# Optimization experiments

Measured on AMD Instinct MI355X. Metric: run time of the kernel, lower is better.

## Reference

```python
import jax, jax.numpy as jnp
import numpy as np

D_MODEL = 768
D_FF = 3072
N_EXPERTS = 4
BATCH, SEQ = 8, 2048


def setup_inputs() -> dict:
    key = jax.random.key(0)
    ks = jax.random.split(key, 8)
    s_in = 1.0 / np.sqrt(D_MODEL)
    s_ff = 1.0 / np.sqrt(D_FF)
    return {
        "hidden_states": jax.random.normal(ks[0], (BATCH, SEQ, D_MODEL), jnp.float32),
        "Wg": jax.random.normal(ks[1], (D_MODEL, N_EXPERTS), jnp.float32) * s_in,
        "bg": jnp.zeros((N_EXPERTS,), jnp.float32),
        "W1": jax.random.normal(ks[2], (N_EXPERTS, D_MODEL, D_FF), jnp.float32) * s_in,
        "b1": jnp.zeros((N_EXPERTS, D_FF), jnp.float32),
        "W2": jax.random.normal(ks[3], (N_EXPERTS, D_FF, D_MODEL), jnp.float32) * s_ff,
        "b2": jnp.zeros((N_EXPERTS, D_MODEL), jnp.float32),
    }


def reference(hidden_states, Wg, bg, W1, b1, W2, b2):
    """Switch-Transformer top-1 MoE FFN (no token dropping).

    router: softmax(x @ Wg + bg); each token goes to argmax expert,
    expert FFN: gelu(x @ W1[e] + b1[e]) @ W2[e] + b2[e],
    output scaled by the winning route probability.
    """
    B, S, D = hidden_states.shape
    xt = hidden_states.reshape(-1, D)                      # [T, D]
    logits = xt @ Wg + bg                                  # [T, E]
    probs = jax.nn.softmax(logits, axis=-1)
    gate = jnp.max(probs, axis=-1)                         # [T]
    route = jnp.argmax(probs, axis=-1)                     # [T] int

    out = jnp.zeros_like(xt)
    for e in range(W1.shape[0]):                           # small fixed expert count
        mask = (route == e).astype(xt.dtype)[:, None]      # [T, 1]
        h = jax.nn.gelu(xt @ W1[e] + b1[e])                # [T, d_ff]
        y = h @ W2[e] + b2[e]                              # [T, D]
        out = out + mask * y
    out = out * gate[:, None]
    return out.reshape(B, S, D)
```

## Files before the change

### kernel.cpp

```cpp
#include <hip/hip_runtime.h>
#include <hip/hip_bf16.h>

#define T_TOK 16384
#define DMODEL 768
#define DFF 3072
#define NEXP 4
#define ROWPAD 512
#define BK 64

typedef __attribute__((ext_vector_type(8))) short bf16x8;
typedef __attribute__((ext_vector_type(4))) float f32x4;

__device__ __forceinline__ void gl_lds16(const void* g, void* l) {
  __builtin_amdgcn_global_load_lds(
      (const __attribute__((address_space(1))) unsigned int*)g,
      (__attribute__((address_space(3))) unsigned int*)l, 16, 0, 0);
}

__device__ __forceinline__ short f2bf(float f) {
  union { float f; unsigned u; } v; v.f = f;
  unsigned r = v.u + 0x7fff + ((v.u >> 16) & 1);
  return (short)(r >> 16);
}

__device__ __forceinline__ float gelu_f(float x) {
  const float c = 0.7978845608028654f;
  float z = c * (x + 0.044715f * x * x * x);
  z = fminf(fmaxf(z, -15.f), 15.f);
  float e = __expf(-2.f * z);
  return 0.5f * x * (1.f + (1.f - e) / (1.f + e));
}


__device__ __forceinline__ int expert_aoff(const int* counts, int e) {
  int off = 0;
  for (int i = 0; i < e; ++i) off += (counts[i] + 127) & ~127;
  return off;
}

__global__ void route_kernel(const float* __restrict__ x, const float* __restrict__ Wg,
                             const float* __restrict__ bg, int* __restrict__ route,
                             float* __restrict__ gate) {
  int t = blockIdx.x * 4 + (threadIdx.x >> 6);
  int l = threadIdx.x & 63;
  const float* xr = x + (size_t)t * DMODEL;
  float s0 = 0.f, s1 = 0.f, s2 = 0.f, s3 = 0.f;
#pragma unroll
  for (int i = 0; i < DMODEL / 64; ++i) {
    int d = l + i * 64;
    float xv = xr[d];
    float4 w = *((const float4*)Wg + d);
    s0 += xv * w.x; s1 += xv * w.y; s2 += xv * w.z; s3 += xv * w.w;
  }
#pragma unroll
  for (int off = 32; off; off >>= 1) {
    s0 += __shfl_xor(s0, off);
    s1 += __shfl_xor(s1, off);
    s2 += __shfl_xor(s2, off);
    s3 += __shfl_xor(s3, off);
  }
  if (l == 0) {
    float lg[4] = { s0 + bg[0], s1 + bg[1], s2 + bg[2], s3 + bg[3] };
    int best = 0; float m = lg[0];
#pragma unroll
    for (int e = 1; e < 4; ++e) if (lg[e] > m) { m = lg[e]; best = e; }
    float s = 0.f;
#pragma unroll
    for (int e = 0; e < 4; ++e) s += __expf(lg[e] - m);
    route[t] = best;
    gate[t] = 1.0f / s;
  }
}

__global__ void bucket_kernel(const int* __restrict__ route, int* __restrict__ counts,
                              int* __restrict__ perm) {
  __shared__ int wcnt[4][NEXP];
  __shared__ int wpre[4][NEXP];
  __shared__ int base[NEXP];
  int tid = threadIdx.x;
  int t = blockIdx.x * 256 + tid;
  int w = tid >> 6, l = tid & 63;
  int r = route[t];
  int lanepre = 0;
  unsigned long long lower = (l == 0) ? 0ull : (~0ull >> (64 - l));
#pragma unroll
  for (int e = 0; e < NEXP; ++e) {
    unsigned long long m = __ballot(r == e);
    if (l == 0) wcnt[w][e] = (int)__popcll(m);
    if (r == e) lanepre = (int)__popcll(m & lower);
  }
  __syncthreads();
  if (tid < NEXP) {
    int s = 0;
#pragma unroll
    for (int ww = 0; ww < 4; ++ww) { wpre[ww][tid] = s; s += wcnt[ww][tid]; }
    base[tid] = atomicAdd(&counts[tid], s);
  }
  __syncthreads();
  int pos = base[r] + wpre[w][r] + lanepre;
  perm[r * T_TOK + pos] = t;
}

__global__ void gather_kernel(const float* __restrict__ x, const int* __restrict__ counts,
                              const int* __restrict__ perm, const float* __restrict__ gate,
                              short* __restrict__ xg, int* __restrict__ tokg,
                              float* __restrict__ gateg) {
  int e = blockIdx.y;
  int cnt = counts[e];
  int pos = blockIdx.x * 8 + (threadIdx.x >> 5);
  if (pos >= cnt) return;
  int off = expert_aoff(counts, e);
  int t = perm[e * T_TOK + pos];
  int g = off + pos;
  int l = threadIdx.x & 31;
  const float* src = x + (size_t)t * DMODEL;
  short* dst = xg + (size_t)g * DMODEL;
  int sw = g & 7;
#pragma unroll
  for (int i = 0; i < 3; ++i) {
    int c = l + 32 * i;
    float4 a = *((const float4*)src + c * 2);
    float4 b = *((const float4*)src + c * 2 + 1);
    bf16x8 v;
    v[0] = f2bf(a.x); v[1] = f2bf(a.y); v[2] = f2bf(a.z); v[3] = f2bf(a.w);
    v[4] = f2bf(b.x); v[5] = f2bf(b.y); v[6] = f2bf(b.z); v[7] = f2bf(b.w);
    int cs = (c & ~7) | ((c & 7) ^ sw);
    *(bf16x8*)(dst + cs * 8) = v;
  }
  if (l == 0) { tokg[g] = t; gateg[g] = gate[t]; }
}

__global__ void transpose_kernel(const float* __restrict__ src, short* __restrict__ dst,
                                 int K, int N) {
  __shared__ float lds[64 * 65];
  int e = blockIdx.z;
  int k0 = blockIdx.x * 64, n0 = blockIdx.y * 64;
  const float* s = src + (size_t)e * K * N;
  short* d = dst + (size_t)e * N * K;
#pragma unroll
  for (int i = 0; i < 16; ++i) {
    int idx = threadIdx.x + i * 256;
    int kk = idx >> 6, nn = idx & 63;
    lds[kk * 65 + nn] = s[(size_t)(k0 + kk) * N + n0 + nn];
  }
  __syncthreads();
#pragma unroll
  for (int i = 0; i < 2; ++i) {
    int cid = threadIdx.x + i * 256;
    int nn = cid >> 3, uu = cid & 7;
    int n = n0 + nn;
    bf16x8 v;
#pragma unroll
    for (int j = 0; j < 8; ++j) v[j] = f2bf(lds[(uu * 8 + j) * 65 + nn]);
    int cs = (k0 >> 3) + (uu ^ (n & 7));
    *(bf16x8*)(d + (size_t)n * K + cs * 8) = v;
  }
}

__device__ __forceinline__ int xcd_chunk(int orig, int nwg) {
  int q = nwg >> 3, r = nwg & 7, xcd = orig & 7;
  return (xcd < r ? xcd * (q + 1) : r * (q + 1) + (xcd - r) * q) + (orig >> 3);
}

__device__ __forceinline__ bool decode_expert(const int* counts, int gm,
                                              int& e, int& off, int& cnt, int& m0) {
  int c0 = counts[0], c1 = counts[1], c2 = counts[2], c3 = counts[3];
  int mb0 = (c0 + 127) >> 7, mb1 = (c1 + 127) >> 7, mb2 = (c2 + 127) >> 7, mb3 = (c3 + 127) >> 7;
  int o1 = (c0 + 127) & ~127, o2 = o1 + ((c1 + 127) & ~127), o3 = o2 + ((c2 + 127) & ~127);
  if (gm < mb0)                        { e = 0; off = 0;  cnt = c0; m0 = gm << 7; return true; }
  if (gm < mb0 + mb1)                  { e = 1; off = o1; cnt = c1; m0 = (gm - mb0) << 7; return true; }
  if (gm < mb0 + mb1 + mb2)            { e = 2; off = o2; cnt = c2; m0 = (gm - mb0 - mb1) << 7; return true; }
  if (gm < mb0 + mb1 + mb2 + mb3)      { e = 3; off = o3; cnt = c3; m0 = (gm - mb0 - mb1 - mb2) << 7; return true; }
  return false;
}

__global__ __launch_bounds__(256, 4)
void gemm1_kernel(const short* __restrict__ xg, const short* __restrict__ w1t,
                  const float* __restrict__ b1, const int* __restrict__ counts,
                  short* __restrict__ h, int FFC, int chunk, int MBG) {
  __shared__ __align__(16) short smem[2 * 128 * 64];
  short* sA = smem;
  short* sB = smem + 128 * 64;
  int L = xcd_chunk(blockIdx.x, gridDim.x);
  int np = L / MBG, gm = L - np * MBG;
  int e, off, cnt, m0;
  if (!decode_expert(counts, gm, e, off, cnt, m0)) return;
  int n0c = np * 128;
  int n0g = chunk * FFC + n0c;

  const char* Abase = (const char*)(xg + (size_t)(off + m0) * DMODEL);
  const char* Bbase = (const char*)(w1t + (size_t)e * DFF * DMODEL + (size_t)n0g * DMODEL);

  int tid = threadIdx.x, wid = tid >> 6, lane = tid & 63;
  int wm = wid >> 1, wn = wid & 1;
  int l15 = lane & 15, u4 = lane >> 4;

  f32x4 acc[4][4];
#pragma unroll
  for (int i = 0; i < 4; ++i)
#pragma unroll
    for (int j = 0; j < 4; ++j) acc[i][j] = (f32x4){0.f, 0.f, 0.f, 0.f};

  for (int kt = 0; kt < DMODEL / BK; ++kt) {
    int kb = kt * 128;
#pragma unroll
    for (int r = 0; r < 4; ++r) {
      int o = wid * 1024 + r * 4096 + lane * 16;
      int row = o >> 7, b = o & 127;
      gl_lds16(Abase + (size_t)row * (DMODEL * 2) + kb + b, (char*)sA + wid * 1024 + r * 4096);
      gl_lds16(Bbase + (size_t)row * (DMODEL * 2) + kb + b, (char*)sB + wid * 1024 + r * 4096);
    }
    __syncthreads();
#pragma unroll
    for (int ks = 0; ks < 2; ++ks) {
      int u = ks * 4 + u4;
      int slot8 = (u ^ (l15 & 7)) << 3;
      bf16x8 af[4], bfr[4];
#pragma unroll
      for (int mi = 0; mi < 4; ++mi)
        af[mi] = *(const bf16x8*)&sA[(wm * 64 + mi * 16 + l15) * 64 + slot8];
#pragma unroll
      for (int ni = 0; ni < 4; ++ni)
        bfr[ni] = *(const bf16x8*)&sB[(wn * 64 + ni * 16 + l15) * 64 + slot8];
#pragma unroll
      for (int mi = 0; mi < 4; ++mi)
#pragma unroll
        for (int ni = 0; ni < 4; ++ni)
          acc[mi][ni] = __builtin_amdgcn_mfma_f32_16x16x32_bf16(af[mi], bfr[ni], acc[mi][ni], 0, 0, 0);
    }
    __syncthreads();
  }

  float bbs[4];
#pragma unroll
  for (int ni = 0; ni < 4; ++ni) bbs[ni] = b1[e * DFF + n0g + wn * 64 + ni * 16 + l15];
  short* bounce = smem;
#pragma unroll
  for (int mi = 0; mi < 4; ++mi)
#pragma unroll
    for (int ni = 0; ni < 4; ++ni) {
      f32x4 v = acc[mi][ni];
      int col = wn * 64 + ni * 16 + l15;
      int c = col >> 3;
#pragma unroll
      for (int qq = 0; qq < 4; ++qq) {
        int rl = wm * 64 + mi * 16 + u4 * 4 + qq;
        int swc = (c & ~7) | ((c & 7) ^ (rl & 7));
        bounce[rl * 128 + swc * 8 + (col & 7)] = f2bf(gelu_f(v[qq] + bbs[ni]));
      }
    }
  __syncthreads();
#pragma unroll
  for (int it = 0; it < 8; ++it) {
    int cc = tid + it * 256;
    int rw = cc >> 4, sl = cc & 15;
    int grow = m0 + rw;
    if (grow < cnt) {
      size_t g = (size_t)off + grow;
      *(bf16x8*)((char*)h + (g * FFC + n0c) * 2 + sl * 16) =
          *(const bf16x8*)((char*)bounce + cc * 16);
    }
  }
}

__global__ __launch_bounds__(512, 4)
void gemm2_kernel(const short* __restrict__ h, const short* __restrict__ w2t,
                  const float* __restrict__ b2, const int* __restrict__ counts,
                  const int* __restrict__ tokg, const float* __restrict__ gateg,
                  float* __restrict__ out, int FFC, int chunk, int nchunks, int MBG) {
  __shared__ __align__(16) short sA[128 * 64];
  __shared__ __align__(16) short sB[256 * 64];
  int L = xcd_chunk(blockIdx.x, gridDim.x);
  int np = L / MBG, gm = L - np * MBG;
  int e, off, cnt, m0;
  if (!decode_expert(counts, gm, e, off, cnt, m0)) return;
  int n0 = np * 256;

  const char* Ar = (const char*)(h + (size_t)(off + m0) * FFC);
  const char* Br = (const char*)(w2t + (size_t)e * DMODEL * DFF + (size_t)n0 * DFF + (size_t)chunk * FFC);

  int tid = threadIdx.x, wid = tid >> 6, lane = tid & 63;
  int wm = wid >> 2, wn = wid & 3;
  int l15 = lane & 15, u4 = lane >> 4;

  f32x4 acc[4][4];
#pragma unroll
  for (int i = 0; i < 4; ++i)
#pragma unroll
    for (int j = 0; j < 4; ++j) acc[i][j] = (f32x4){0.f, 0.f, 0.f, 0.f};

  for (int kt = 0; kt < FFC / BK; ++kt) {
    int kb = kt * 128;
#pragma unroll
    for (int p = 0; p < 2; ++p) {
      int cc = tid + p * 512;
      int row = cc >> 3, b = (cc & 7) * 16;
      gl_lds16(Ar + (size_t)row * (FFC * 2) + kb + b, (char*)sA + (wid * 64 + p * 512) * 16);
    }
#pragma unroll
    for (int p = 0; p < 4; ++p) {
      int cc = tid + p * 512;
      int row = cc >> 3, b = (cc & 7) * 16;
      gl_lds16(Br + (size_t)row * (DFF * 2) + kb + b, (char*)sB + (wid * 64 + p * 512) * 16);
    }
    __syncthreads();
#pragma unroll
    for (int ks = 0; ks < 2; ++ks) {
      int u = ks * 4 + u4;
      int slot8 = (u ^ (l15 & 7)) << 3;
      bf16x8 af[4], bfr[4];
#pragma unroll
      for (int mi = 0; mi < 4; ++mi)
        af[mi] = *(const bf16x8*)&sA[(wm * 64 + mi * 16 + l15) * 64 + slot8];
#pragma unroll
      for (int ni = 0; ni < 4; ++ni)
        bfr[ni] = *(const bf16x8*)&sB[(wn * 64 + ni * 16 + l15) * 64 + slot8];
#pragma unroll
      for (int mi = 0; mi < 4; ++mi)
#pragma unroll
        for (int ni = 0; ni < 4; ++ni)
          acc[mi][ni] = __builtin_amdgcn_mfma_f32_16x16x32_bf16(af[mi], bfr[ni], acc[mi][ni], 0, 0, 0);
    }
    __syncthreads();
  }

#pragma unroll
  for (int ni = 0; ni < 4; ++ni) {
    int colg = n0 + wn * 64 + ni * 16 + l15;
    float bb = b2[e * DMODEL + colg];
#pragma unroll
    for (int mi = 0; mi < 4; ++mi) {
      f32x4 v = acc[mi][ni];
#pragma unroll
      for (int qq = 0; qq < 4; ++qq) {
        int ml = m0 + wm * 64 + mi * 16 + u4 * 4 + qq;
        if (ml < cnt) {
          int g = off + ml;
          float* op = out + (size_t)tokg[g] * DMODEL + colg;
          float pv = v[qq];
          if (chunk == 0 && nchunks > 1) {
            *op = pv;
          } else if (chunk < nchunks - 1) {
            *op += pv;
          } else {
            float prev = (nchunks > 1) ? *op : 0.f;
            *op = (prev + pv + bb) * gateg[g];
          }
        }
      }
    }
  }
}

extern "C" void kernel_launch(void* const* d_in, const int* in_sizes, int n_in,
                              void* d_out, int out_size, void* d_ws, size_t ws_size,
                              hipStream_t stream) {
  (void)in_sizes; (void)n_in; (void)out_size;
  const float* x  = (const float*)d_in[0];
  const float* Wg = (const float*)d_in[1];
  const float* bg = (const float*)d_in[2];
  const float* W1 = (const float*)d_in[3];
  const float* b1 = (const float*)d_in[4];
  const float* W2 = (const float*)d_in[5];
  const float* b2 = (const float*)d_in[6];
  float* out = (float*)d_out;
  char* ws = (char*)d_ws;

  size_t cur = 0;
  auto take = [&](size_t bytes) -> size_t {
    cur = (cur + 255) & ~(size_t)255;
    size_t r = cur; cur += bytes; return r;
  };
  size_t o_counts = take(64);
  size_t o_perm  = take((size_t)NEXP * T_TOK * 4);
  size_t o_route = take((size_t)T_TOK * 4);
  size_t o_gate  = take((size_t)T_TOK * 4);
  size_t o_tokg  = take((size_t)(T_TOK + ROWPAD) * 4);
  size_t o_gateg = take((size_t)(T_TOK + ROWPAD) * 4);
  size_t o_w1t   = take((size_t)NEXP * DFF * DMODEL * 2);
  size_t o_w2t   = take((size_t)NEXP * DMODEL * DFF * 2);
  size_t o_xg    = take((size_t)(T_TOK + ROWPAD) * DMODEL * 2);
  cur = (cur + 255) & ~(size_t)255;
  size_t o_h = cur;

  int FFC = 384;
  const int cands[4] = {3072, 1536, 768, 384};
  for (int i = 0; i < 4; ++i) {
    if (o_h + (size_t)(T_TOK + ROWPAD) * cands[i] * 2 <= ws_size) { FFC = cands[i]; break; }
  }

  int*   counts = (int*)(ws + o_counts);
  int*   perm   = (int*)(ws + o_perm);
  int*   routeb = (int*)(ws + o_route);
  float* gate   = (float*)(ws + o_gate);
  int*   tokg   = (int*)(ws + o_tokg);
  float* gateg  = (float*)(ws + o_gateg);
  short* w1t    = (short*)(ws + o_w1t);
  short* w2t    = (short*)(ws + o_w2t);
  short* xg     = (short*)(ws + o_xg);
  short* hbuf   = (short*)(ws + o_h);

  hipMemsetAsync(counts, 0, 64, stream);
  route_kernel<<<T_TOK / 4, 256, 0, stream>>>(x, Wg, bg, routeb, gate);
  bucket_kernel<<<T_TOK / 256, 256, 0, stream>>>(routeb, counts, perm);
  transpose_kernel<<<dim3(DMODEL / 64, DFF / 64, NEXP), 256, 0, stream>>>(W1, w1t, DMODEL, DFF);
  transpose_kernel<<<dim3(DFF / 64, DMODEL / 64, NEXP), 256, 0, stream>>>(W2, w2t, DFF, DMODEL);
  gather_kernel<<<dim3(T_TOK / 8, NEXP), 256, 0, stream>>>(x, counts, perm, gate, xg, tokg, gateg);

  int NC = DFF / FFC;
  int MBG = T_TOK / 128 + (NEXP - 1);
  int NB2 = DMODEL / 256;
  for (int c = 0; c < NC; ++c) {
    int NB1 = FFC / 128;
    gemm1_kernel<<<NB1 * MBG, 256, 0, stream>>>(xg, w1t, b1, counts, hbuf, FFC, c, MBG);
    gemm2_kernel<<<NB2 * MBG, 512, 0, stream>>>(hbuf, w2t, b2, counts, tokg, gateg, out, FFC, c, NC, MBG);
  }
}
```

Before: 292.5 us.

## Enlarge gemm1 to 256x256 tiles with double-buffered LDS pipeline and 256-row expert padding

Measured after the change: 344.9 us. 17.9% more time.

```diff
diff --git a/kernel.cpp b/kernel.cpp
--- a/kernel.cpp
+++ b/kernel.cpp
@@ -5,7 +5,7 @@
 #define DMODEL 768
 #define DFF 3072
 #define NEXP 4
-#define ROWPAD 512
+#define ROWPAD 1024
 #define BK 64
 
 typedef __attribute__((ext_vector_type(8))) short bf16x8;
@@ -29,13 +29,6 @@
   z = fminf(fmaxf(z, -15.f), 15.f);
   float e = __expf(-2.f * z);
   return 0.5f * x * (1.f + (1.f - e) / (1.f + e));
-}
-
-
-__device__ __forceinline__ int expert_aoff(const int* counts, int e) {
-  int off = 0;
-  for (int i = 0; i < e; ++i) off += (counts[i] + 127) & ~127;
-  return off;
 }
 
 __global__ void route_kernel(const float* __restrict__ x, const float* __restrict__ Wg,
@@ -101,20 +94,34 @@
   perm[r * T_TOK + pos] = t;
 }
 
+__device__ __forceinline__ int expert_aoff256(const int* counts, int e) {
+  int off = 0;
+  for (int i = 0; i < e; ++i) off += (counts[i] + 255) & ~255;
+  return off;
+}
+
 __global__ void gather_kernel(const float* __restrict__ x, const int* __restrict__ counts,
                               const int* __restrict__ perm, const float* __restrict__ gate,
                               short* __restrict__ xg, int* __restrict__ tokg,
                               float* __restrict__ gateg) {
   int e = blockIdx.y;
   int cnt = counts[e];
+  int cntp = (cnt + 255) & ~255;
   int pos = blockIdx.x * 8 + (threadIdx.x >> 5);
-  if (pos >= cnt) return;
-  int off = expert_aoff(counts, e);
-  int t = perm[e * T_TOK + pos];
+  if (pos >= cntp) return;
+  int off = expert_aoff256(counts, e);
   int g = off + pos;
   int l = threadIdx.x & 31;
+  short* dst = xg + (size_t)g * DMODEL;
+  if (pos >= cnt) {
+    bf16x8 z = (bf16x8){0,0,0,0,0,0,0,0};
+#pragma unroll
+    for (int i = 0; i < 3; ++i) *(bf16x8*)(dst + (l + 32 * i) * 8) = z;
+    if (l == 0) { tokg[g] = 0; gateg[g] = 0.f; }
+    return;
+  }
+  int t = perm[e * T_TOK + pos];
   const float* src = x + (size_t)t * DMODEL;
-  short* dst = xg + (size_t)g * DMODEL;
   int sw = g & 7;
 #pragma unroll
   for (int i = 0; i < 3; ++i) {
@@ -162,103 +169,133 @@
   return (xcd < r ? xcd * (q + 1) : r * (q + 1) + (xcd - r) * q) + (orig >> 3);
 }
 
-__device__ __forceinline__ bool decode_expert(const int* counts, int gm,
-                                              int& e, int& off, int& cnt, int& m0) {
+template <int THL>
+__device__ __forceinline__ bool decode_t(const int* counts, int gm,
+                                         int& e, int& off, int& cnt, int& m0) {
   int c0 = counts[0], c1 = counts[1], c2 = counts[2], c3 = counts[3];
-  int mb0 = (c0 + 127) >> 7, mb1 = (c1 + 127) >> 7, mb2 = (c2 + 127) >> 7, mb3 = (c3 + 127) >> 7;
-  int o1 = (c0 + 127) & ~127, o2 = o1 + ((c1 + 127) & ~127), o3 = o2 + ((c2 + 127) & ~127);
-  if (gm < mb0)                        { e = 0; off = 0;  cnt = c0; m0 = gm << 7; return true; }
-  if (gm < mb0 + mb1)                  { e = 1; off = o1; cnt = c1; m0 = (gm - mb0) << 7; return true; }
-  if (gm < mb0 + mb1 + mb2)            { e = 2; off = o2; cnt = c2; m0 = (gm - mb0 - mb1) << 7; return true; }
-  if (gm < mb0 + mb1 + mb2 + mb3)      { e = 3; off = o3; cnt = c3; m0 = (gm - mb0 - mb1 - mb2) << 7; return true; }
+  const int thm = (1 << THL) - 1;
+  int mb0 = (c0 + thm) >> THL, mb1 = (c1 + thm) >> THL, mb2 = (c2 + thm) >> THL, mb3 = (c3 + thm) >> THL;
+  int o1 = (c0 + 255) & ~255, o2 = o1 + ((c1 + 255) & ~255), o3 = o2 + ((c2 + 255) & ~255);
+  if (gm < mb0)                    { e = 0; off = 0;  cnt = c0; m0 = gm << THL; return true; }
+  if (gm < mb0 + mb1)              { e = 1; off = o1; cnt = c1; m0 = (gm - mb0) << THL; return true; }
+  if (gm < mb0 + mb1 + mb2)        { e = 2; off = o2; cnt = c2; m0 = (gm - mb0 - mb1) << THL; return true; }
+  if (gm < mb0 + mb1 + mb2 + mb3)  { e = 3; off = o3; cnt = c3; m0 = (gm - mb0 - mb1 - mb2) << THL; return true; }
   return false;
 }
 
-__global__ __launch_bounds__(256, 4)
+__global__ __launch_bounds__(512, 2)
 void gemm1_kernel(const short* __restrict__ xg, const short* __restrict__ w1t,
                   const float* __restrict__ b1, const int* __restrict__ counts,
                   short* __restrict__ h, int FFC, int chunk, int MBG) {
-  __shared__ __align__(16) short smem[2 * 128 * 64];
-  short* sA = smem;
-  short* sB = smem + 128 * 64;
+  __shared__ __align__(16) short LA[2][2][128 * 64];
+  __shared__ __align__(16) short LB[2][2][128 * 64];
   int L = xcd_chunk(blockIdx.x, gridDim.x);
   int np = L / MBG, gm = L - np * MBG;
   int e, off, cnt, m0;
-  if (!decode_expert(counts, gm, e, off, cnt, m0)) return;
-  int n0c = np * 128;
+  if (!decode_t<8>(counts, gm, e, off, cnt, m0)) return;
+  int n0c = np * 256;
   int n0g = chunk * FFC + n0c;
 
-  const char* Abase = (const char*)(xg + (size_t)(off + m0) * DMODEL);
-  const char* Bbase = (const char*)(w1t + (size_t)e * DFF * DMODEL + (size_t)n0g * DMODEL);
+  const char* Ab = (const char*)(xg + (size_t)(off + m0) * DMODEL);
+  const char* Bb = (const char*)(w1t + (size_t)e * DFF * DMODEL + (size_t)n0g * DMODEL);
+  const int AS = DMODEL * 2;
 
   int tid = threadIdx.x, wid = tid >> 6, lane = tid & 63;
-  int wm = wid >> 1, wn = wid & 1;
+  int wm = wid >> 2, wn = wid & 3;
   int l15 = lane & 15, u4 = lane >> 4;
-
-  f32x4 acc[4][4];
-#pragma unroll
-  for (int i = 0; i < 4; ++i)
+  int bh = wn >> 1, brb = (wn & 1) * 64;
+  int srow = tid >> 3, scol = (tid & 7) * 16;
+
+  f32x4 acc[8][4];
+#pragma unroll
+  for (int i = 0; i < 8; ++i)
 #pragma unroll
     for (int j = 0; j < 4; ++j) acc[i][j] = (f32x4){0.f, 0.f, 0.f, 0.f};
 
-  for (int kt = 0; kt < DMODEL / BK; ++kt) {
-    int kb = kt * 128;
-#pragma unroll
-    for (int r = 0; r < 4; ++r) {
-      int o = wid * 1024 + r * 4096 + lane * 16;
-      int row = o >> 7, b = o & 127;
-      gl_lds16(Abase + (size_t)row * (DMODEL * 2) + kb + b, (char*)sA + wid * 1024 + r * 4096);
-      gl_lds16(Bbase + (size_t)row * (DMODEL * 2) + kb + b, (char*)sB + wid * 1024 + r * 4096);
-    }
-    __syncthreads();
-#pragma unroll
-    for (int ks = 0; ks < 2; ++ks) {
-      int u = ks * 4 + u4;
-      int slot8 = (u ^ (l15 & 7)) << 3;
-      bf16x8 af[4], bfr[4];
-#pragma unroll
-      for (int mi = 0; mi < 4; ++mi)
-        af[mi] = *(const bf16x8*)&sA[(wm * 64 + mi * 16 + l15) * 64 + slot8];
-#pragma unroll
-      for (int ni = 0; ni < 4; ++ni)
-        bfr[ni] = *(const bf16x8*)&sB[(wn * 64 + ni * 16 + l15) * 64 + slot8];
-#pragma unroll
-      for (int mi = 0; mi < 4; ++mi)
-#pragma unroll
-        for (int ni = 0; ni < 4; ++ni)
-          acc[mi][ni] = __builtin_amdgcn_mfma_f32_16x16x32_bf16(af[mi], bfr[ni], acc[mi][ni], 0, 0, 0);
-    }
-    __syncthreads();
-  }
-
+#define STG1(tt) { int kb = (tt) * 128; int sl = (tt) & 1;                            \
+    _Pragma("unroll") for (int hh = 0; hh < 2; ++hh)                                  \
+    _Pragma("unroll") for (int p = 0; p < 2; ++p) {                                   \
+      int row = hh * 128 + srow + p * 64;                                             \
+      gl_lds16(Ab + (size_t)row * AS + kb + scol, (char*)&LA[sl][hh][0] + (tid + p * 512) * 16); \
+      gl_lds16(Bb + (size_t)row * AS + kb + scol, (char*)&LB[sl][hh][0] + (tid + p * 512) * 16); \
+    } }
+
+  const int NT = DMODEL / BK;
+  STG1(0);
+  asm volatile("s_waitcnt vmcnt(0)" ::: "memory");
+  __builtin_amdgcn_s_barrier();
+
+  bf16x8 a[4][2], b[2][2];
+  for (int t = 0; t < NT; ++t) {
+    int s = t & 1;
+    const short* pa = &LA[s][wm][l15 * 64];
+    const short* pb = &LB[s][bh][(brb + l15) * 64];
+#pragma unroll
+    for (int q = 0; q < 4; ++q) {
+      const int mh = q >> 1, nh = q & 1;
+      if (nh == 0) {
+#pragma unroll
+        for (int mi = 0; mi < 4; ++mi)
+#pragma unroll
+          for (int ks = 0; ks < 2; ++ks)
+            a[mi][ks] = *(const bf16x8*)(pa + (mh * 4 + mi) * 16 * 64 + (((ks * 4 + u4) ^ (l15 & 7)) << 3));
+      }
+#pragma unroll
+      for (int ni = 0; ni < 2; ++ni)
+#pragma unroll
+        for (int ks = 0; ks < 2; ++ks)
+          b[ni][ks] = *(const bf16x8*)(pb + (nh * 2 + ni) * 16 * 64 + (((ks * 4 + u4) ^ (l15 & 7)) << 3));
+      if (q == 0 && t + 1 < NT) STG1(t + 1);
+      if (q == 3) asm volatile("s_waitcnt vmcnt(0)" ::: "memory");
+      __builtin_amdgcn_sched_barrier(0);
+      __builtin_amdgcn_s_barrier();
+      __builtin_amdgcn_s_setprio(1);
+#pragma unroll
+      for (int ks = 0; ks < 2; ++ks)
+#pragma unroll
+        for (int mi = 0; mi < 4; ++mi)
+#pragma unroll
+          for (int ni = 0; ni < 2; ++ni)
+            acc[mh * 4 + mi][nh * 2 + ni] = __builtin_amdgcn_mfma_f32_16x16x32_bf16(
+                a[mi][ks], b[ni][ks], acc[mh * 4 + mi][nh * 2 + ni], 0, 0, 0);
+      __builtin_amdgcn_s_setprio(0);
+      __builtin_amdgcn_s_barrier();
+    }
+  }
+#undef STG1
+
+  __syncthreads();
+  short* loS = &LA[0][0][0];
+  short* hiS = &LB[0][0][0];
   float bbs[4];
 #pragma unroll
   for (int ni = 0; ni < 4; ++ni) bbs[ni] = b1[e * DFF + n0g + wn * 64 + ni * 16 + l15];
-  short* bounce = smem;
-#pragma unroll
-  for (int mi = 0; mi < 4; ++mi)
+  short* half = (wm == 0) ? loS : hiS;
+#pragma unroll
+  for (int mi = 0; mi < 8; ++mi) {
 #pragma unroll
     for (int ni = 0; ni < 4; ++ni) {
       f32x4 v = acc[mi][ni];
       int col = wn * 64 + ni * 16 + l15;
       int c = col >> 3;
 #pragma unroll
-      for (int qq = 0; qq < 4; ++qq) {
-        int rl = wm * 64 + mi * 16 + u4 * 4 + qq;
-        int swc = (c & ~7) | ((c & 7) ^ (rl & 7));
-        bounce[rl * 128 + swc * 8 + (col & 7)] = f2bf(gelu_f(v[qq] + bbs[ni]));
+      for (int r = 0; r < 4; ++r) {
+        int rr = mi * 16 + u4 * 4 + r;
+        int swc = (c & ~7) | ((c & 7) ^ (rr & 7));
+        half[rr * 256 + swc * 8 + (col & 7)] = f2bf(gelu_f(v[r] + bbs[ni]));
       }
     }
+  }
   __syncthreads();
 #pragma unroll
-  for (int it = 0; it < 8; ++it) {
-    int cc = tid + it * 256;
-    int rw = cc >> 4, sl = cc & 15;
+  for (int it = 0; it < 16; ++it) {
+    int cc = tid + it * 512;
+    int rw = cc >> 5, sl = cc & 31;
     int grow = m0 + rw;
     if (grow < cnt) {
       size_t g = (size_t)off + grow;
-      *(bf16x8*)((char*)h + (g * FFC + n0c) * 2 + sl * 16) =
-          *(const bf16x8*)((char*)bounce + cc * 16);
+      const short* src = ((rw < 128) ? loS : hiS) + (rw & 127) * 256 + sl * 8;
+      *(bf16x8*)((char*)h + (g * FFC + n0c) * 2 + sl * 16) = *(const bf16x8*)src;
     }
   }
 }
@@ -273,7 +310,7 @@
   int L = xcd_chunk(blockIdx.x, gridDim.x);
   int np = L / MBG, gm = L - np * MBG;
   int e, off, cnt, m0;
-  if (!decode_expert(counts, gm, e, off, cnt, m0)) return;
+  if (!decode_t<7>(counts, gm, e, off, cnt, m0)) return;
   int n0 = np * 256;
 
   const char* Ar = (const char*)(h + (size_t)(off + m0) * FFC);
@@ -383,9 +420,9 @@
   cur = (cur + 255) & ~(size_t)255;
   size_t o_h = cur;
 
-  int FFC = 384;
-  const int cands[4] = {3072, 1536, 768, 384};
-  for (int i = 0; i < 4; ++i) {
+  int FFC = 256;
+  const int cands[5] = {3072, 1536, 768, 512, 256};
+  for (int i = 0; i < 5; ++i) {
     if (o_h + (size_t)(T_TOK + ROWPAD) * cands[i] * 2 <= ws_size) { FFC = cands[i]; break; }
   }
 
@@ -405,14 +442,15 @@
   bucket_kernel<<<T_TOK / 256, 256, 0, stream>>>(routeb, counts, perm);
   transpose_kernel<<<dim3(DMODEL / 64, DFF / 64, NEXP), 256, 0, stream>>>(W1, w1t, DMODEL, DFF);
   transpose_kernel<<<dim3(DFF / 64, DMODEL / 64, NEXP), 256, 0, stream>>>(W2, w2t, DFF, DMODEL);
-  gather_kernel<<<dim3(T_TOK / 8, NEXP), 256, 0, stream>>>(x, counts, perm, gate, xg, tokg, gateg);
+  gather_kernel<<<dim3(T_TOK / 8 + 32, NEXP), 256, 0, stream>>>(x, counts, perm, gate, xg, tokg, gateg);
 
   int NC = DFF / FFC;
-  int MBG = T_TOK / 128 + (NEXP - 1);
+  int MBG1 = T_TOK / 256 + (NEXP - 1);
+  int MBG2 = T_TOK / 128 + (NEXP - 1);
   int NB2 = DMODEL / 256;
   for (int c = 0; c < NC; ++c) {
-    int NB1 = FFC / 128;
-    gemm1_kernel<<<NB1 * MBG, 256, 0, stream>>>(xg, w1t, b1, counts, hbuf, FFC, c, MBG);
-    gemm2_kernel<<<NB2 * MBG, 512, 0, stream>>>(hbuf, w2t, b2, counts, tokg, gateg, out, FFC, c, NC, MBG);
-  }
-}
+    int NB1 = FFC / 256;
+    gemm1_kernel<<<NB1 * MBG1, 512, 0, stream>>>(xg, w1t, b1, counts, hbuf, FFC, c, MBG1);
+    gemm2_kernel<<<NB2 * MBG2, 512, 0, stream>>>(hbuf, w2t, b2, counts, tokg, gateg, out, FFC, c, NC, MBG2);
+  }
+}
```

## Store hidden activations and W2 in contiguous pre-swizzled 64x64 tiles

Applied to the files above, without the earlier changes.

New measurement: 274.7 us. 1.06x faster.

```diff
diff --git a/kernel.cpp b/kernel.cpp
--- a/kernel.cpp
+++ b/kernel.cpp
@@ -7,6 +7,7 @@
 #define NEXP 4
 #define ROWPAD 512
 #define BK 64
+#define MBLK_MAX (T_TOK / 128 + NEXP)
 
 typedef __attribute__((ext_vector_type(8))) short bf16x8;
 typedef __attribute__((ext_vector_type(4))) float f32x4;
@@ -157,6 +158,34 @@
   }
 }
 
+__global__ void transpose_tiled_kernel(const float* __restrict__ src, short* __restrict__ dst,
+                                       int K, int N) {
+  __shared__ float lds[64 * 65];
+  int e = blockIdx.z;
+  int k0 = blockIdx.x * 64, n0 = blockIdx.y * 64;
+  const float* s = src + (size_t)e * K * N;
+#pragma unroll
+  for (int i = 0; i < 16; ++i) {
+    int idx = threadIdx.x + i * 256;
+    int kk = idx >> 6, nn = idx & 63;
+    lds[kk * 65 + nn] = s[(size_t)(k0 + kk) * N + n0 + nn];
+  }
+  __syncthreads();
+  size_t tile = ((size_t)e * (K >> 6) + (k0 >> 6)) * (N >> 6) + (n0 >> 6);
+  short* d = dst + tile * 4096;
+#pragma unroll
+  for (int i = 0; i < 2; ++i) {
+    int cid = threadIdx.x + i * 256;
+    int nn = cid >> 3, uu = cid & 7;
+    int n = n0 + nn;
+    bf16x8 v;
+#pragma unroll
+    for (int j = 0; j < 8; ++j) v[j] = f2bf(lds[(uu * 8 + j) * 65 + nn]);
+    int cs = uu ^ (n & 7);
+    *(bf16x8*)(d + nn * 64 + cs * 8) = v;
+  }
+}
+
 __device__ __forceinline__ int xcd_chunk(int orig, int nwg) {
   int q = nwg >> 3, r = nwg & 7, xcd = orig & 7;
   return (xcd < r ? xcd * (q + 1) : r * (q + 1) + (xcd - r) * q) + (orig >> 3);
@@ -250,16 +279,14 @@
       }
     }
   __syncthreads();
+  int mblk = (off + m0) >> 7;
+  size_t tb = ((size_t)mblk * (FFC >> 6) + (n0c >> 6)) * 8192;
 #pragma unroll
   for (int it = 0; it < 8; ++it) {
     int cc = tid + it * 256;
     int rw = cc >> 4, sl = cc & 15;
-    int grow = m0 + rw;
-    if (grow < cnt) {
-      size_t g = (size_t)off + grow;
-      *(bf16x8*)((char*)h + (g * FFC + n0c) * 2 + sl * 16) =
-          *(const bf16x8*)((char*)bounce + cc * 16);
-    }
+    size_t dsto = tb + (size_t)(sl >> 3) * 8192 + rw * 64 + (sl & 7) * 8;
+    *(bf16x8*)(h + dsto) = *(const bf16x8*)((char*)bounce + cc * 16);
   }
 }
 
@@ -276,8 +303,11 @@
   if (!decode_expert(counts, gm, e, off, cnt, m0)) return;
   int n0 = np * 256;
 
-  const char* Ar = (const char*)(h + (size_t)(off + m0) * FFC);
-  const char* Br = (const char*)(w2t + (size_t)e * DMODEL * DFF + (size_t)n0 * DFF + (size_t)chunk * FFC);
+  int mblk = (off + m0) >> 7;
+  const char* Atile = (const char*)(h + (size_t)mblk * (FFC >> 6) * 8192);
+  const int N64 = DMODEL >> 6;
+  const char* Btile = (const char*)(w2t + (((size_t)e * (DFF >> 6)) * N64 + (np << 2)) * 4096);
+  const int ktg0 = chunk * (FFC >> 6);
 
   int tid = threadIdx.x, wid = tid >> 6, lane = tid & 63;
   int wm = wid >> 2, wn = wid & 3;
@@ -290,18 +320,17 @@
     for (int j = 0; j < 4; ++j) acc[i][j] = (f32x4){0.f, 0.f, 0.f, 0.f};
 
   for (int kt = 0; kt < FFC / BK; ++kt) {
-    int kb = kt * 128;
+    const char* at = Atile + (size_t)kt * 16384;
+    const char* bt = Btile + (size_t)(ktg0 + kt) * (N64 * 8192);
 #pragma unroll
     for (int p = 0; p < 2; ++p) {
       int cc = tid + p * 512;
-      int row = cc >> 3, b = (cc & 7) * 16;
-      gl_lds16(Ar + (size_t)row * (FFC * 2) + kb + b, (char*)sA + (wid * 64 + p * 512) * 16);
+      gl_lds16(at + cc * 16, (char*)sA + (wid * 64 + p * 512) * 16);
     }
 #pragma unroll
     for (int p = 0; p < 4; ++p) {
       int cc = tid + p * 512;
-      int row = cc >> 3, b = (cc & 7) * 16;
-      gl_lds16(Br + (size_t)row * (DFF * 2) + kb + b, (char*)sB + (wid * 64 + p * 512) * 16);
+      gl_lds16(bt + cc * 16, (char*)sB + (wid * 64 + p * 512) * 16);
     }
     __syncthreads();
 #pragma unroll
@@ -386,7 +415,8 @@
   int FFC = 384;
   const int cands[4] = {3072, 1536, 768, 384};
   for (int i = 0; i < 4; ++i) {
-    if (o_h + (size_t)(T_TOK + ROWPAD) * cands[i] * 2 <= ws_size) { FFC = cands[i]; break; }
+    size_t hbytes = (size_t)MBLK_MAX * (cands[i] >> 6) * 16384;
+    if (o_h + hbytes <= ws_size) { FFC = cands[i]; break; }
   }
 
   int*   counts = (int*)(ws + o_counts);
@@ -404,7 +434,7 @@
   route_kernel<<<T_TOK / 4, 256, 0, stream>>>(x, Wg, bg, routeb, gate);
   bucket_kernel<<<T_TOK / 256, 256, 0, stream>>>(routeb, counts, perm);
   transpose_kernel<<<dim3(DMODEL / 64, DFF / 64, NEXP), 256, 0, stream>>>(W1, w1t, DMODEL, DFF);
-  transpose_kernel<<<dim3(DFF / 64, DMODEL / 64, NEXP), 256, 0, stream>>>(W2, w2t, DFF, DMODEL);
+  transpose_tiled_kernel<<<dim3(DFF / 64, DMODEL / 64, NEXP), 256, 0, stream>>>(W2, w2t, DFF, DMODEL);
   gather_kernel<<<dim3(T_TOK / 8, NEXP), 256, 0, stream>>>(x, counts, perm, gate, xg, tokg, gateg);
 
   int NC = DFF / FFC;
```
